# Optimization experiments

Measured on AMD Instinct MI355X. Metric: run time of the kernel, lower is better.

The kernel has to match this reference:

```python
import jax, jax.numpy as jnp
import numpy as np

B, T, H, W, C = 2, 8, 20, 36, 512
NH = 4
HD = C // NH
WS = (5, 9)
EXP = (2, 4)              # window_size // 2
KP = (5, 9)               # focal unfold kernel for level k=0
PADP = (2, 4)
T2T_K, T2T_S, T2T_P = (7, 7), (3, 3), (3, 3)
FFN_HD = 1960
NWH, NWW = H // WS[0], W // WS[1]   # 4, 4
WAREA = WS[0] * WS[1]               # 45


def _valid_ind_rolled():
    wh, ww = WS
    eh, ew = EXP
    m = np.ones((4, wh, ww), np.float32)
    m[0, :wh - eh, :ww - ew] = 0   # tl
    m[1, :wh - eh, ew:] = 0        # tr
    m[2, eh:, :ww - ew] = 0        # bl
    m[3, eh:, ew:] = 0             # br
    return jnp.asarray(np.nonzero(m.reshape(-1))[0])

VALID_ROLLED = _valid_ind_rolled()  # (120,)


def unfold(x, k, s, p):
    # x: (N, Cc, Hh, Ww) -> (N, Cc*kh*kw, L); matches torch.nn.Unfold layout (c slowest).
    N, Cc, Hh, Ww = x.shape
    kh, kw = k; sh, sw = s; ph, pw = p
    xp = jnp.pad(x, ((0, 0), (0, 0), (ph, ph), (pw, pw)))
    oh = (Hh + 2 * ph - kh) // sh + 1
    ow = (Ww + 2 * pw - kw) // sw + 1
    cols = [xp[:, :, i:i + oh * sh:sh, j:j + ow * sw:sw]
            for i in range(kh) for j in range(kw)]
    patches = jnp.stack(cols, axis=2)            # (N, Cc, kh*kw, oh, ow)
    return patches.reshape(N, Cc * kh * kw, oh * ow)


def fold(patches, out_hw, k, s, p):
    # inverse of unfold (overlap-add), matches torch F.fold.
    N = patches.shape[0]
    kh, kw = k; sh, sw = s; ph, pw = p
    Hh, Ww = out_hw
    oh = (Hh + 2 * ph - kh) // sh + 1
    ow = (Ww + 2 * pw - kw) // sw + 1
    Cc = patches.shape[1] // (kh * kw)
    pr = patches.reshape(N, Cc, kh, kw, oh, ow)
    out = jnp.zeros((N, Cc, Hh + 2 * ph, Ww + 2 * pw), patches.dtype)
    for i in range(kh):
        for j in range(kw):
            out = out.at[:, :, i:i + oh * sh:sh, j:j + ow * sw:sw].add(pr[:, :, i, j])
    return out[:, :, ph:ph + Hh, pw:pw + Ww]


def layer_norm(x, g, b):
    mu = jnp.mean(x, -1, keepdims=True)
    var = jnp.var(x, -1, keepdims=True)
    return (x - mu) * jax.lax.rsqrt(var + 1e-5) * g + b


def win_part(x):
    # (B,T,H,W,C) -> (B*nW, T*wh*ww, C)
    b = x.shape[0]
    x = x.reshape(b, T, NWH, WS[0], NWW, WS[1], C)
    return x.transpose(0, 2, 4, 1, 3, 5, 6).reshape(-1, T * WAREA, C)


def to_heads(w):
    return w.reshape(-1, T, WAREA, NH, HD).transpose(0, 3, 1, 2, 4).reshape(-1, NH, T * WAREA, HD)


def block_forward(x, g1, be1, wqkv, bqkv, wproj, bproj, wpool, bpool, g2, be2, w1, bf1, w2, bf2, out_h, out_w):
    shortcut = x
    xn = layer_norm(x, g1, be1)

    # ---- coarser (pooled) focal level, k=0 (focal_level=2) ----
    wnr = xn.reshape(B, T, NWH, WS[0], NWW, WS[1], C).transpose(0, 2, 4, 1, 3, 5, 6)
    wnr = wnr.reshape(B, NWH, NWW, T, WAREA, C)
    pooled = jnp.einsum('bhwtnc,n->bhwtc', wnr, wpool) + bpool   # (B,NWH,NWW,T,C)

    # ---- window attention ----
    qkv = xn @ wqkv + bqkv                                       # (B,T,H,W,3C)
    q, k, v = jnp.split(qkv, 3, axis=-1)
    qw = to_heads(win_part(q)) * (HD ** -0.5)
    kw_, vw = to_heads(win_part(k)), to_heads(win_part(v))

    def rolled(t):
        parts = []
        for sh, sw in ((-EXP[0], -EXP[1]), (-EXP[0], EXP[1]), (EXP[0], -EXP[1]), (EXP[0], EXP[1])):
            r = jnp.roll(t, (sh, sw), axis=(2, 3))
            parts.append(win_part(r).reshape(-1, T, WAREA, NH, HD))
        cat = jnp.concatenate(parts, axis=2)                     # (B*nW, T, 4*warea, NH, HD)
        cat = jnp.take(cat.transpose(0, 3, 1, 2, 4), VALID_ROLLED, axis=3)
        return cat.reshape(-1, NH, T * VALID_ROLLED.shape[0], HD)

    k_rolled = jnp.concatenate([kw_, rolled(k)], axis=2)         # (B*nW, NH, T*165, HD)
    v_rolled = jnp.concatenate([vw, rolled(v)], axis=2)

    # pooled keys/values via focal unfold
    xp = pooled.transpose(0, 3, 1, 2, 4)                          # (B,T,NWH,NWW,C)
    qkv_p = xp @ wqkv + bqkv
    kp, vp = qkv_p[..., C:2 * C], qkv_p[..., 2 * C:]

    def unfold_kv(t):
        t = t.transpose(0, 1, 4, 2, 3).reshape(B * T, C, NWH, NWW)
        u = unfold(t, KP, (1, 1), PADP)                           # (B*T, C*45, L)
        L = u.shape[-1]
        u = u.reshape(B, T, C, KP[0], KP[1], L).transpose(0, 5, 1, 3, 4, 2)
        u = u.reshape(B * L, T, KP[0] * KP[1], NH, HD).transpose(0, 3, 1, 2, 4)
        return u.reshape(B * L, NH, T * KP[0] * KP[1], HD)

    k_all = jnp.concatenate([k_rolled, unfold_kv(kp)], axis=2)
    v_all = jnp.concatenate([v_rolled, unfold_kv(vp)], axis=2)

    attn = jnp.einsum('wnqd,wnkd->wnqk', qw, k_all)               # (B*nW, NH, T*45, N)

    # validity mask for pooled context (zero-padded unfold positions -> -100)
    ones = jnp.ones((T, 1, NWH, NWW), x.dtype)
    um = unfold(ones, KP, (1, 1), PADP)                           # (T, 45, L)
    L = um.shape[-1]
    mvals = jnp.where(um.reshape(T, KP[0] * KP[1], L).transpose(2, 0, 1).reshape(L, -1) == 0,
                      jnp.asarray(-100.0, x.dtype), jnp.asarray(0.0, x.dtype))
    n_rolled = k_rolled.shape[2]
    mask_cols = jnp.concatenate([jnp.zeros((L, n_rolled), x.dtype), mvals], axis=1)
    attn = attn + jnp.tile(mask_cols, (B, 1))[:, None, None, :]

    attn = jax.nn.softmax(attn, axis=-1)
    out = jnp.einsum('wnqk,wnkd->wnqd', attn, v_all)
    out = out.transpose(0, 2, 1, 3).reshape(-1, T * WAREA, C) @ wproj + bproj

    # window reverse + residual
    out = out.reshape(B, NWH, NWW, T, WS[0], WS[1], C)
    out = out.transpose(0, 3, 1, 4, 2, 5, 6).reshape(B, T, H, W, C)
    x = shortcut + out

    # ---- FusionFeedForward (fold/unfold re-normalized MLP) ----
    y = layer_norm(x, g2, be2).reshape(B, T * H * W, C)
    h = y @ w1 + bf1                                              # (B, n, 1960)
    nvec = ((out_h + 2 * T2T_P[0] - T2T_K[0]) // T2T_S[0] + 1) * \
           ((out_w + 2 * T2T_P[1] - T2T_K[1]) // T2T_S[1] + 1)
    bt = (B * T * H * W) // nvec
    norm_p = jnp.ones((bt, T2T_K[0] * T2T_K[1], nvec), x.dtype)
    norm_f = fold(norm_p, (out_h, out_w), T2T_K, T2T_S, T2T_P)    # (bt,1,out_h,out_w)
    h_f = fold(h.reshape(bt, nvec, FFN_HD).transpose(0, 2, 1), (out_h, out_w), T2T_K, T2T_S, T2T_P)
    h = unfold(h_f / norm_f, T2T_K, T2T_S, T2T_P).transpose(0, 2, 1).reshape(B, T * H * W, FFN_HD)
    h = jax.nn.gelu(h, approximate=False) @ w2 + bf2
    return x + h.reshape(B, T, H, W, C)


def setup_inputs() -> dict:
    key = jax.random.key(0)
    ks = jax.random.split(key, 8)
    s = 0.02
    return dict(
        x=jax.random.normal(ks[0], (B, T, H, W, C), jnp.float32),
        g1=jnp.ones((C,), jnp.float32),
        be1=jnp.zeros((C,), jnp.float32),
        wqkv=jax.random.normal(ks[1], (C, 3 * C), jnp.float32) * s,
        bqkv=jnp.zeros((3 * C,), jnp.float32),
        wproj=jax.random.normal(ks[2], (C, C), jnp.float32) * s,
        bproj=jnp.zeros((C,), jnp.float32),
        wpool=jnp.full((WAREA,), 1.0 / WAREA, jnp.float32),
        bpool=jnp.zeros((1,), jnp.float32),
        g2=jnp.ones((C,), jnp.float32),
        be2=jnp.zeros((C,), jnp.float32),
        w1=jax.random.normal(ks[3], (C, FFN_HD), jnp.float32) * s,
        bf1=jnp.zeros((FFN_HD,), jnp.float32),
        w2=jax.random.normal(ks[4], (FFN_HD, C), jnp.float32) * s,
        bf2=jnp.zeros((C,), jnp.float32),
        out_h=60,
        out_w=108,
    )


def reference(x, g1, be1, wqkv, bqkv, wproj, bproj, wpool, bpool, g2, be2, w1, bf1, w2, bf2, out_h, out_w):
    return block_forward(x, g1, be1, wqkv, bqkv, wproj, bproj, wpool, bpool,
                         g2, be2, w1, bf1, w2, bf2, out_h, out_w)
```

## Files before the change

### kernel.cpp

```cpp
#include <hip/hip_runtime.h>
#include <hip/hip_bf16.h>
#include <math.h>

typedef __hip_bfloat16 bf16;
typedef __attribute__((ext_vector_type(8))) short bf16x8;
typedef __attribute__((ext_vector_type(4))) float f32x4;

#define DEVI __device__ __forceinline__

#define C_ 512
#define NH_ 4
#define NTOK 11520
#define NKEY 1680
#define NRK 120
#define FFN_ 1960
#define POOLED_FLAG 0x40000000

DEVI float bfu(unsigned u) { return __uint_as_float(u << 16); }
DEVI float ldf(const bf16* p) { return __bfloat162float(*p); }
DEVI float ldf(const float* p) { return *p; }
DEVI void stw(bf16* p, float v) { *p = __float2bfloat16(v); }
DEVI void stw(float* p, float v) { *p = v; }
DEVI unsigned short f2bs(float f) { bf16 h = __float2bfloat16(f); return *(unsigned short*)&h; }
DEVI unsigned pk2(float a, float b) {
  return (unsigned)f2bs(a) | ((unsigned)f2bs(b) << 16);
}

template <int DT> DEVI float ldw(const void* p, size_t i) {
  if (DT == 0) return __bfloat162float(((const bf16*)p)[i]);
  else         return ((const float*)p)[i];
}

DEVI void gload_lds16(const void* g, void* l) {
  __builtin_amdgcn_global_load_lds(
      (const __attribute__((address_space(1))) void*)g,
      (__attribute__((address_space(3))) void*)l, 16, 0, 0);
}

__global__ void k_detect(const void* __restrict__ g1, int* __restrict__ flag) {
  if (threadIdx.x == 0) {
    const unsigned short* p = (const unsigned short*)g1;
    *flag = (p[0] == 0x3F80u) ? 0 : 1;
  }
}

__global__ void k_prep(int* __restrict__ table) {
  if (threadIdx.x == 0) {
    int cnt = 0;
    for (int p = 0; p < 4; p++)
      for (int wi = 0; wi < 5; wi++)
        for (int wj = 0; wj < 9; wj++) {
          bool invalid;
          if (p == 0)      invalid = (wi < 3) && (wj < 5);
          else if (p == 1) invalid = (wi < 3) && (wj >= 4);
          else if (p == 2) invalid = (wi >= 2) && (wj < 5);
          else             invalid = (wi >= 2) && (wj >= 4);
          if (!invalid) table[cnt++] = p * 45 + wi * 9 + wj;
        }
  }
}

__global__ void k_ksrc(const int* __restrict__ vtab, int* __restrict__ ksrc) {
  int idx = blockIdx.x * 256 + threadIdx.x;
  if (idx >= 32 * NKEY) return;
  int w = idx / NKEY, j = idx % NKEY;
  int b = w >> 4, nh = (w >> 2) & 3, nw = w & 3;
  int val;
  if (j < 360) {
    int t = j / 45, pos = j % 45, wi = pos / 9, wj2 = pos % 9;
    val = ((b * 8 + t) * 20 + nh * 5 + wi) * 36 + nw * 9 + wj2;
  } else if (j < 1320) {
    int jj = j - 360;
    int t = jj / 120, r = jj % 120;
    int id = vtab[r];
    int p = id / 45, pos = id % 45, wi = pos / 9, wj2 = pos % 9;
    int sh = (p < 2) ? -2 : 2;
    int sw = (p & 1) ? 4 : -4;
    int hh = nh * 5 + wi - sh;
    if (hh < 0) hh += 20; else if (hh >= 20) hh -= 20;
    int ww2 = nw * 9 + wj2 - sw;
    if (ww2 < 0) ww2 += 36; else if (ww2 >= 36) ww2 -= 36;
    val = ((b * 8 + t) * 20 + hh) * 36 + ww2;
  } else {
    int jj = j - 1320;
    int t = jj / 45, kidx = jj % 45, ki = kidx / 9, kj = kidx % 9;
    int snh = nh + ki - 2, snw = nw + kj - 4;
    if (snh < 0 || snh >= 4 || snw < 0 || snw >= 4) val = -1;
    else val = POOLED_FLAG | ((b * 8 + t) * 16 + snh * 4 + snw);
  }
  ksrc[idx] = val;
}

template <int DT>
__global__ void k_wcvt(const int* __restrict__ dflag, const void* __restrict__ in,
                       bf16* __restrict__ out, int K, int N, int Npad) {
  if (*dflag != DT) return;
  int idx = blockIdx.x * 256 + threadIdx.x;
  if (idx >= Npad * K) return;
  int n = idx / K, k = idx % K;
  float v = (n < N) ? ldw<DT>(in, (size_t)k * N + n) : 0.f;
  out[idx] = __float2bfloat16(v);
}

template <int DT>
__global__ void k_bcvt(const int* __restrict__ dflag, const void* __restrict__ in,
                       float* __restrict__ out, int n) {
  if (*dflag != DT) return;
  int i = blockIdx.x * 256 + threadIdx.x;
  if (i < n) out[i] = ldw<DT>(in, i);
}

template <int DT, typename InT>
__global__ void k_ln(const int* __restrict__ dflag, const InT* __restrict__ xin,
                     const void* __restrict__ g, const void* __restrict__ be,
                     bf16* __restrict__ out) {
  if (*dflag != DT) return;
  const int tok = blockIdx.x;
  const int tid = threadIdx.x;
  const size_t base = (size_t)tok * C_;
  float v0 = ldf(xin + base + tid);
  float v1 = ldf(xin + base + tid + 256);
  float s = v0 + v1, ss = v0 * v0 + v1 * v1;
#pragma unroll
  for (int o = 32; o; o >>= 1) { s += __shfl_xor(s, o); ss += __shfl_xor(ss, o); }
  __shared__ float sh[10];
  const int lane = tid & 63, wv = tid >> 6;
  if (lane == 0) { sh[wv] = s; sh[4 + wv] = ss; }
  __syncthreads();
  if (tid == 0) {
    float a = sh[0] + sh[1] + sh[2] + sh[3];
    float q = sh[4] + sh[5] + sh[6] + sh[7];
    float mu = a * (1.0f / C_);
    float var = q * (1.0f / C_) - mu * mu;
    sh[8] = mu; sh[9] = rsqrtf(fmaxf(var, 0.f) + 1e-5f);
  }
  __syncthreads();
  float mu = sh[8], inv = sh[9];
  stw(out + base + tid,
      (v0 - mu) * inv * ldw<DT>(g, tid) + ldw<DT>(be, tid));
  stw(out + base + tid + 256,
      (v1 - mu) * inv * ldw<DT>(g, tid + 256) + ldw<DT>(be, tid + 256));
}

template <int DT>
__global__ void k_pool(const int* __restrict__ dflag, const bf16* __restrict__ xn,
                       const void* __restrict__ wpool, const void* __restrict__ bpool,
                       float* __restrict__ pooled) {
  if (*dflag != DT) return;
  int idx = blockIdx.x * blockDim.x + threadIdx.x;
  if (idx >= 256 * C_) return;
  int c = idx & (C_ - 1);
  int fw = idx >> 9;
  int nw = fw & 3, nh = (fw >> 2) & 3;
  int bt = fw >> 4;
  float acc = ldw<DT>(bpool, 0);
  for (int wi = 0; wi < 5; wi++) {
    int hh = nh * 5 + wi;
    const bf16* base = xn + (((size_t)(bt * 20 + hh)) * 36 + nw * 9) * C_ + c;
    for (int wj = 0; wj < 9; wj++)
      acc += __bfloat162float(base[(size_t)wj * C_]) * ldw<DT>(wpool, wi * 9 + wj);
  }
  pooled[idx] = acc;
}

template <int DT>
__global__ void k_gemm_small(const int* __restrict__ dflag, const float* __restrict__ A,
                             const void* __restrict__ Bw, const void* __restrict__ bias,
                             float* __restrict__ Cc) {
  if (*dflag != DT) return;
  int n = blockIdx.x * blockDim.x + threadIdx.x;
  int m = blockIdx.y;
  if (n >= 1536) return;
  float acc = ldw<DT>(bias, n);
  const float* a = A + (size_t)m * C_;
  for (int k = 0; k < C_; k++)
    acc += a[k] * ldw<DT>(Bw, (size_t)k * 1536 + n);
  Cc[(size_t)m * 1536 + n] = acc;
}

template <int DT, int RES, typename OutT>
__global__ __launch_bounds__(256) void k_gemm_m(const int* __restrict__ dflag,
                                                const bf16* __restrict__ A,
                                                const bf16* __restrict__ Bt,
                                                const float* __restrict__ bias,
                                                const void* __restrict__ resid,
                                                OutT* __restrict__ out,
                                                int M, int N, int K) {
  if (dflag && *dflag != DT) return;
  __shared__ __align__(16) unsigned short As[128 * 32];
  __shared__ __align__(16) unsigned short Bs[128 * 32];
  const int tid = threadIdx.x;
  const int lane = tid & 63, wid = tid >> 6;
  const int r15 = lane & 15, quad = lane >> 4;
  const int wm = wid >> 1, wn = wid & 1;
  const int m0 = blockIdx.y * 128, n0 = blockIdx.x * 128;

  f32x4 acc[4][4];
#pragma unroll
  for (int i = 0; i < 4; i++)
#pragma unroll
    for (int j = 0; j < 4; j++)
#pragma unroll
      for (int e = 0; e < 4; e++) acc[i][j][e] = 0.f;

  const int lrow = lane >> 2, lcol = (lane & 3) * 8;

  for (int k0 = 0; k0 < K; k0 += 32) {
    int rem = K - k0;
    if (rem >= 32) {
      const bf16* ga = A + (size_t)(m0 + wid * 32 + lrow) * K + k0 + lcol;
      gload_lds16(ga, &As[wid * 1024]);
      gload_lds16(ga + (size_t)16 * K, &As[wid * 1024 + 512]);
      const bf16* gb = Bt + (size_t)(n0 + wid * 32 + lrow) * K + k0 + lcol;
      gload_lds16(gb, &Bs[wid * 1024]);
      gload_lds16(gb + (size_t)16 * K, &Bs[wid * 1024 + 512]);
    } else {
      int r = tid >> 2, c = (tid & 3) * 8;
      uint4 z = make_uint4(0, 0, 0, 0);
      uint4 a0 = z, a1 = z, b0 = z, b1 = z;
      if (c < rem) {
        a0 = *(const uint4*)(A + (size_t)(m0 + r) * K + k0 + c);
        a1 = *(const uint4*)(A + (size_t)(m0 + r + 64) * K + k0 + c);
        b0 = *(const uint4*)(Bt + (size_t)(n0 + r) * K + k0 + c);
        b1 = *(const uint4*)(Bt + (size_t)(n0 + r + 64) * K + k0 + c);
      }
      *(uint4*)&As[r * 32 + c] = a0;
      *(uint4*)&As[(r + 64) * 32 + c] = a1;
      *(uint4*)&Bs[r * 32 + c] = b0;
      *(uint4*)&Bs[(r + 64) * 32 + c] = b1;
    }
    __syncthreads();

    bf16x8 af[4], bfr[4];
#pragma unroll
    for (int mf = 0; mf < 4; mf++)
      af[mf] = *(const bf16x8*)&As[(wm * 64 + mf * 16 + r15) * 32 + quad * 8];
#pragma unroll
    for (int nf = 0; nf < 4; nf++)
      bfr[nf] = *(const bf16x8*)&Bs[(wn * 64 + nf * 16 + r15) * 32 + quad * 8];
#pragma unroll
    for (int mf = 0; mf < 4; mf++)
#pragma unroll
      for (int nf = 0; nf < 4; nf++)
        acc[mf][nf] = __builtin_amdgcn_mfma_f32_16x16x32_bf16(af[mf], bfr[nf],
                                                              acc[mf][nf], 0, 0, 0);
    __syncthreads();
  }

#pragma unroll
  for (int nf = 0; nf < 4; nf++) {
    int n = n0 + wn * 64 + nf * 16 + r15;
    if (n >= N) continue;
    float bv = bias[n];
#pragma unroll
    for (int mf = 0; mf < 4; mf++) {
      int mb = m0 + wm * 64 + mf * 16 + quad * 4;
#pragma unroll
      for (int e = 0; e < 4; e++) {
        size_t off = (size_t)(mb + e) * N + n;
        float v = acc[mf][nf][e] + bv;
        if (RES == 1) v += ldw<DT>(resid, off);
        else if (RES == 2) v += ((const float*)resid)[off];
        stw(out + off, v);
      }
    }
  }
}

#define KT 64
#define KPAD 136
#define VPAD 72
__global__ __launch_bounds__(256) void k_attn_m(const bf16* __restrict__ qkv,
                                                const float* __restrict__ qkvp,
                                                const int* __restrict__ ksrc,
                                                bf16* __restrict__ ao) {
  __shared__ int ks_l[NKEY];
  __shared__ __align__(16) unsigned short ktl[KT * KPAD];
  __shared__ __align__(16) unsigned short vtl[128 * VPAD];
  __shared__ __align__(16) unsigned short ptl[4 * 16 * VPAD];
  __shared__ float maskv[KT];

  const int tid = threadIdx.x;
  const int lane = tid & 63, wid = tid >> 6;
  const int r15 = lane & 15, quad = lane >> 4;
  const int w = blockIdx.x, qt = blockIdx.y, n = blockIdx.z;
  const int b = w >> 4, nh = (w >> 2) & 3, nw = w & 3;
  const unsigned short* qkvs = (const unsigned short*)qkv;

  for (int j = tid; j < NKEY; j += 256) ks_l[j] = ksrc[w * NKEY + j];

  bf16x8 qf[4];
  {
    int qw = qt * 64 + wid * 16 + r15;
    int qc2 = qw < 360 ? qw : 359;
    int t = qc2 / 45, pos = qc2 % 45, wi = pos / 9, wj = pos % 9;
    int tok = ((b * 8 + t) * 20 + nh * 5 + wi) * 36 + nw * 9 + wj;
    const unsigned short* qp = qkvs + (size_t)tok * 1536 + n * 128 + quad * 8;
#pragma unroll
    for (int c = 0; c < 4; c++)
      qf[c] = *(const bf16x8*)(qp + c * 32);
  }

  f32x4 of[8];
#pragma unroll
  for (int nt = 0; nt < 8; nt++)
#pragma unroll
    for (int e = 0; e < 4; e++) of[nt][e] = 0.f;
  float m_[4], l_[4];
#pragma unroll
  for (int e = 0; e < 4; e++) { m_[e] = -1e30f; l_[e] = 0.f; }

  unsigned short* ptw = &ptl[wid * 16 * VPAD];
  __syncthreads();

  const int kr = tid >> 2, kp = tid & 3;
  const int vr = lane, vp = wid;
  uint4 kreg[4], vreg[4];
  float mreg = -30000.f;

  auto load_tile = [&](int j0) {
    int cnt = NKEY - j0; if (cnt > KT) cnt = KT;
    {
      int s0 = (kr < cnt) ? ks_l[j0 + kr] : -1;
      mreg = (s0 < 0) ? -30000.f : 0.f;
      if (s0 < 0) {
        kreg[0] = kreg[1] = kreg[2] = kreg[3] = make_uint4(0, 0, 0, 0);
      } else if (s0 & POOLED_FLAG) {
        const float* kf = qkvp + (size_t)(s0 & 0x3FFFFFFF) * 1536 + 512 + n * 128 + kp * 32;
#pragma unroll
        for (int i = 0; i < 4; i++) {
          float4 f0 = ((const float4*)kf)[2 * i], f1 = ((const float4*)kf)[2 * i + 1];
          kreg[i] = make_uint4(pk2(f0.x, f0.y), pk2(f0.z, f0.w),
                               pk2(f1.x, f1.y), pk2(f1.z, f1.w));
        }
      } else {
        const uint4* kq = (const uint4*)(qkvs + (size_t)s0 * 1536 + 512 + n * 128 + kp * 32);
#pragma unroll
        for (int i = 0; i < 4; i++) kreg[i] = kq[i];
      }
    }
    {
      int s1 = (vr < cnt) ? ks_l[j0 + vr] : -1;
      if (s1 < 0) {
        vreg[0] = vreg[1] = vreg[2] = vreg[3] = make_uint4(0, 0, 0, 0);
      } else if (s1 & POOLED_FLAG) {
        const float* vf = qkvp + (size_t)(s1 & 0x3FFFFFFF) * 1536 + 1024 + n * 128 + vp * 32;
#pragma unroll
        for (int i = 0; i < 4; i++) {
          float4 f0 = ((const float4*)vf)[2 * i], f1 = ((const float4*)vf)[2 * i + 1];
          vreg[i] = make_uint4(pk2(f0.x, f0.y), pk2(f0.z, f0.w),
                               pk2(f1.x, f1.y), pk2(f1.z, f1.w));
        }
      } else {
        const uint4* vq = (const uint4*)(qkvs + (size_t)s1 * 1536 + 1024 + n * 128 + vp * 32);
#pragma unroll
        for (int i = 0; i < 4; i++) vreg[i] = vq[i];
      }
    }
  };

  auto store_tile = [&]() {
    if (kp == 0) maskv[kr] = mreg;
#pragma unroll
    for (int i = 0; i < 4; i++)
      *(uint4*)&ktl[kr * KPAD + kp * 32 + i * 8] = kreg[i];
#pragma unroll
    for (int i = 0; i < 4; i++) {
      uint4 u = vreg[i];
      int d0 = vp * 32 + i * 8;
      vtl[(d0 + 0) * VPAD + vr] = (unsigned short)(u.x & 0xFFFFu);
      vtl[(d0 + 1) * VPAD + vr] = (unsigned short)(u.x >> 16);
      vtl[(d0 + 2) * VPAD + vr] = (unsigned short)(u.y & 0xFFFFu);
      vtl[(d0 + 3) * VPAD + vr] = (unsigned short)(u.y >> 16);
      vtl[(d0 + 4) * VPAD + vr] = (unsigned short)(u.z & 0xFFFFu);
      vtl[(d0 + 5) * VPAD + vr] = (unsigned short)(u.z >> 16);
      vtl[(d0 + 6) * VPAD + vr] = (unsigned short)(u.w & 0xFFFFu);
      vtl[(d0 + 7) * VPAD + vr] = (unsigned short)(u.w >> 16);
    }
  };

  load_tile(0);
  store_tile();
  __syncthreads();

  int j0 = 0;
  while (true) {
    int nxt = j0 + KT;
    if (nxt < NKEY) load_tile(nxt);

    f32x4 sf[4];
#pragma unroll
    for (int ft = 0; ft < 4; ft++)
#pragma unroll
      for (int e = 0; e < 4; e++) sf[ft][e] = 0.f;
#pragma unroll
    for (int kc = 0; kc < 4; kc++) {
      bf16x8 a = qf[kc];
#pragma unroll
      for (int ft = 0; ft < 4; ft++) {
        bf16x8 bb = *(const bf16x8*)&ktl[(ft * 16 + r15) * KPAD + kc * 32 + quad * 8];
        sf[ft] = __builtin_amdgcn_mfma_f32_16x16x32_bf16(a, bb, sf[ft], 0, 0, 0);
      }
    }
    const float scl = 0.088388347648318447f;
#pragma unroll
    for (int ft = 0; ft < 4; ft++) {
      float mk = maskv[ft * 16 + r15];
#pragma unroll
      for (int e = 0; e < 4; e++) sf[ft][e] = sf[ft][e] * scl + mk;
    }
    float tm[4], rs[4];
#pragma unroll
    for (int e = 0; e < 4; e++) {
      float v = fmaxf(fmaxf(sf[0][e], sf[1][e]), fmaxf(sf[2][e], sf[3][e]));
#pragma unroll
      for (int o = 1; o < 16; o <<= 1) v = fmaxf(v, __shfl_xor(v, o));
      tm[e] = v;
    }
#pragma unroll
    for (int e = 0; e < 4; e++) {
      float mn = fmaxf(m_[e], tm[e]);
      float alpha = __expf(m_[e] - mn);
      m_[e] = mn;
      rs[e] = 0.f;
#pragma unroll
      for (int ft = 0; ft < 4; ft++) {
        float pv = __expf(sf[ft][e] - mn);
        rs[e] += pv;
        ptw[(quad * 4 + e) * VPAD + ft * 16 + r15] = f2bs(pv);
      }
#pragma unroll
      for (int o = 1; o < 16; o <<= 1) rs[e] += __shfl_xor(rs[e], o);
      l_[e] = l_[e] * alpha + rs[e];
#pragma unroll
      for (int nt = 0; nt < 8; nt++) of[nt][e] *= alpha;
    }
#pragma unroll
    for (int kc = 0; kc < 2; kc++) {
      bf16x8 pa = *(const bf16x8*)&ptw[r15 * VPAD + kc * 32 + quad * 8];
#pragma unroll
      for (int nt = 0; nt < 8; nt++) {
        bf16x8 vb = *(const bf16x8*)&vtl[(nt * 16 + r15) * VPAD + kc * 32 + quad * 8];
        of[nt] = __builtin_amdgcn_mfma_f32_16x16x32_bf16(pa, vb, of[nt], 0, 0, 0);
      }
    }

    if (nxt >= NKEY) break;
    __syncthreads();
    store_tile();
    __syncthreads();
    j0 = nxt;
  }

#pragma unroll
  for (int e = 0; e < 4; e++) {
    int qw = qt * 64 + wid * 16 + quad * 4 + e;
    if (qw >= 360) continue;
    float inv = 1.0f / l_[e];
    int t = qw / 45, pos = qw % 45, wi = pos / 9, wj = pos % 9;
    int tok = ((b * 8 + t) * 20 + nh * 5 + wi) * 36 + nw * 9 + wj;
    bf16* op = ao + (size_t)tok * 512 + n * 128 + r15;
#pragma unroll
    for (int nt = 0; nt < 8; nt++)
      stw(op + nt * 16, of[nt][e] * inv);
  }
}

__global__ void k_fold(const bf16* __restrict__ h1, float* __restrict__ hf) {
  int idx = blockIdx.x * 256 + threadIdx.x;
  if (idx >= 16 * 40 * 60 * 108) return;
  int x = idx % 108;
  int tmp = idx / 108;
  int y = tmp % 60; tmp /= 60;
  int c = tmp % 40;
  int bt = tmp / 40;
  float sum = 0.f;
  int cnt = 0;
  for (int ki = y % 3; ki < 7; ki += 3) {
    int num = y + 3 - ki;
    if (num < 0) continue;
    int oh = num / 3;
    if (oh >= 20) continue;
    for (int kj = x % 3; kj < 7; kj += 3) {
      int num2 = x + 3 - kj;
      if (num2 < 0) continue;
      int ow = num2 / 3;
      if (ow >= 36) continue;
      sum += __bfloat162float(
          h1[(size_t)(bt * 720 + oh * 36 + ow) * FFN_ + c * 49 + ki * 7 + kj]);
      cnt++;
    }
  }
  hf[idx] = sum / (float)cnt;
}

__global__ void k_unfold_gelu(const float* __restrict__ hf, bf16* __restrict__ h2) {
  int idx = blockIdx.x * 256 + threadIdx.x;
  if (idx >= NTOK * FFN_) return;
  int f = idx % FFN_;
  int token = idx / FFN_;
  int c = f / 49, k = f % 49, ki = k / 7, kj = k % 7;
  int bt = token / 720, vec = token % 720;
  int oh = vec / 36, ow = vec % 36;
  int y = oh * 3 + ki - 3, x = ow * 3 + kj - 3;
  float v = 0.f;
  if (y >= 0 && y < 60 && x >= 0 && x < 108)
    v = hf[((size_t)(bt * 40 + c) * 60 + y) * 108 + x];
  float g = 0.5f * v * (1.0f + erff(v * 0.70710678118654752f));
  stw(h2 + idx, g);
}

extern "C" void kernel_launch(void* const* d_in, const int* in_sizes, int n_in,
                              void* d_out, int out_size, void* d_ws, size_t ws_size,
                              hipStream_t stream) {
  (void)in_sizes; (void)n_in; (void)out_size; (void)ws_size;
  const void* x     = d_in[0];
  const void* g1    = d_in[1];
  const void* be1   = d_in[2];
  const void* wqkv  = d_in[3];
  const void* bqkv  = d_in[4];
  const void* wproj = d_in[5];
  const void* bproj = d_in[6];
  const void* wpool = d_in[7];
  const void* bpool = d_in[8];
  const void* g2    = d_in[9];
  const void* be2   = d_in[10];
  const void* w1    = d_in[11];
  const void* bf1   = d_in[12];
  const void* w2    = d_in[13];
  const void* bf2   = d_in[14];

  char* ws = (char*)d_ws;
  size_t off = 0;
  auto alloc = [&](size_t bytes) -> void* {
    void* p = ws + off;
    off += (bytes + 255) & ~(size_t)255;
    return p;
  };

  int*   dflag  = (int*)  alloc(256);
  int*   vtab   = (int*)  alloc(NRK * sizeof(int));
  int*   ksrc   = (int*)  alloc((size_t)32 * NKEY * sizeof(int));
  bf16*  buf2   = (bf16*) alloc((size_t)NTOK * FFN_ * 2);
  float* pooled = (float*)alloc((size_t)256 * C_ * 4);
  float* qkvp   = (float*)alloc((size_t)256 * 1536 * 4);
  float* x2     = (float*)alloc((size_t)NTOK * C_ * 4);
  float* hf     = (float*)alloc((size_t)16 * 40 * 60 * 108 * 4);
  bf16*  wqkv_t = (bf16*) alloc((size_t)1536 * 512 * 2);
  bf16*  wproj_t= (bf16*) alloc((size_t)512 * 512 * 2);
  bf16*  w1_t   = (bf16*) alloc((size_t)2048 * 512 * 2);
  bf16*  w2_t   = (bf16*) alloc((size_t)512 * FFN_ * 2);
  float* bqkv_f = (float*)alloc(1536 * 4);
  float* bproj_f= (float*)alloc(512 * 4);
  float* bf1_f  = (float*)alloc(FFN_ * 4);
  float* bf2_f  = (float*)alloc(512 * 4);

  bf16* buf1 = (bf16*)d_out;
  bf16* xn = buf1;
  bf16* ao = buf1;
  bf16* y  = buf1;
  bf16* qkv = buf2;
  bf16* h1  = buf2;

  k_detect<<<1, 64, 0, stream>>>(g1, dflag);
  k_prep<<<1, 64, 0, stream>>>(vtab);
  k_ksrc<<<(32 * NKEY) / 256, 256, 0, stream>>>(vtab, ksrc);

  k_wcvt<0><<<(1536 * 512) / 256, 256, 0, stream>>>(dflag, wqkv, wqkv_t, 512, 1536, 1536);
  k_wcvt<1><<<(1536 * 512) / 256, 256, 0, stream>>>(dflag, wqkv, wqkv_t, 512, 1536, 1536);
  k_wcvt<0><<<(512 * 512) / 256, 256, 0, stream>>>(dflag, wproj, wproj_t, 512, 512, 512);
  k_wcvt<1><<<(512 * 512) / 256, 256, 0, stream>>>(dflag, wproj, wproj_t, 512, 512, 512);
  k_wcvt<0><<<(2048 * 512) / 256, 256, 0, stream>>>(dflag, w1, w1_t, 512, FFN_, 2048);
  k_wcvt<1><<<(2048 * 512) / 256, 256, 0, stream>>>(dflag, w1, w1_t, 512, FFN_, 2048);
  k_wcvt<0><<<(512 * FFN_ + 255) / 256, 256, 0, stream>>>(dflag, w2, w2_t, FFN_, 512, 512);
  k_wcvt<1><<<(512 * FFN_ + 255) / 256, 256, 0, stream>>>(dflag, w2, w2_t, FFN_, 512, 512);
  k_bcvt<0><<<6, 256, 0, stream>>>(dflag, bqkv, bqkv_f, 1536);
  k_bcvt<1><<<6, 256, 0, stream>>>(dflag, bqkv, bqkv_f, 1536);
  k_bcvt<0><<<2, 256, 0, stream>>>(dflag, bproj, bproj_f, 512);
  k_bcvt<1><<<2, 256, 0, stream>>>(dflag, bproj, bproj_f, 512);
  k_bcvt<0><<<8, 256, 0, stream>>>(dflag, bf1, bf1_f, FFN_);
  k_bcvt<1><<<8, 256, 0, stream>>>(dflag, bf1, bf1_f, FFN_);
  k_bcvt<0><<<2, 256, 0, stream>>>(dflag, bf2, bf2_f, 512);
  k_bcvt<1><<<2, 256, 0, stream>>>(dflag, bf2, bf2_f, 512);

  k_ln<0, bf16><<<NTOK, 256, 0, stream>>>(dflag, (const bf16*)x, g1, be1, xn);
  k_ln<1, float><<<NTOK, 256, 0, stream>>>(dflag, (const float*)x, g1, be1, xn);

  k_pool<0><<<512, 256, 0, stream>>>(dflag, xn, wpool, bpool, pooled);
  k_pool<1><<<512, 256, 0, stream>>>(dflag, xn, wpool, bpool, pooled);

  k_gemm_m<0, 0, bf16><<<dim3(12, 90), 256, 0, stream>>>(
      nullptr, xn, wqkv_t, bqkv_f, nullptr, qkv, NTOK, 1536, 512);

  k_gemm_small<0><<<dim3(6, 256), 256, 0, stream>>>(dflag, pooled, wqkv, bqkv, qkvp);
  k_gemm_small<1><<<dim3(6, 256), 256, 0, stream>>>(dflag, pooled, wqkv, bqkv, qkvp);

  k_attn_m<<<dim3(32, 6, NH_), 256, 0, stream>>>(qkv, qkvp, ksrc, ao);

  k_gemm_m<0, 1, float><<<dim3(4, 90), 256, 0, stream>>>(
      dflag, ao, wproj_t, bproj_f, x, x2, NTOK, 512, 512);
  k_gemm_m<1, 1, float><<<dim3(4, 90), 256, 0, stream>>>(
      dflag, ao, wproj_t, bproj_f, x, x2, NTOK, 512, 512);

  k_ln<0, float><<<NTOK, 256, 0, stream>>>(dflag, x2, g2, be2, y);
  k_ln<1, float><<<NTOK, 256, 0, stream>>>(dflag, x2, g2, be2, y);

  k_gemm_m<0, 0, bf16><<<dim3(16, 90), 256, 0, stream>>>(
      nullptr, y, w1_t, bf1_f, nullptr, h1, NTOK, FFN_, 512);

  k_fold<<<(16 * 40 * 60 * 108) / 256, 256, 0, stream>>>(h1, hf);

  k_unfold_gelu<<<(NTOK * FFN_) / 256, 256, 0, stream>>>(hf, h1);

  k_gemm_m<0, 2, bf16><<<dim3(4, 90), 256, 0, stream>>>(
      dflag, h1, w2_t, bf2_f, x2, (bf16*)d_out, NTOK, 512, FFN_);
  k_gemm_m<1, 2, float><<<dim3(4, 90), 256, 0, stream>>>(
      dflag, h1, w2_t, bf2_f, x2, (float*)d_out, NTOK, 512, FFN_);
}
```

Baseline: 636.4 us.

## Merge dtype-duplicated launches, tile weight transpose, use 64x64 GEMM for N=512

Replaces the per-dtype template kernel pairs with single kernels that branch on the runtime dtype flag, which roughly halves the number of launches. Weight conversion becomes one batched kernel that transposes through a shared-memory tile, so both global reads and writes are coalesced, and bias conversion becomes one kernel. The two N=512 GEMMs (proj and FFN down) move to a new 64x64-tile MFMA kernel with four times as many blocks, to fill the CUs better. The cost is runtime branching in the store path and less data reuse per block in the smaller-tile GEMM.

```diff
diff --git a/kernel.cpp b/kernel.cpp
--- a/kernel.cpp
+++ b/kernel.cpp
@@ -17,18 +17,13 @@
 #define POOLED_FLAG 0x40000000
 
 DEVI float bfu(unsigned u) { return __uint_as_float(u << 16); }
-DEVI float ldf(const bf16* p) { return __bfloat162float(*p); }
-DEVI float ldf(const float* p) { return *p; }
 DEVI void stw(bf16* p, float v) { *p = __float2bfloat16(v); }
-DEVI void stw(float* p, float v) { *p = v; }
 DEVI unsigned short f2bs(float f) { bf16 h = __float2bfloat16(f); return *(unsigned short*)&h; }
 DEVI unsigned pk2(float a, float b) {
   return (unsigned)f2bs(a) | ((unsigned)f2bs(b) << 16);
 }
-
-template <int DT> DEVI float ldw(const void* p, size_t i) {
-  if (DT == 0) return __bfloat162float(((const bf16*)p)[i]);
-  else         return ((const float*)p)[i];
+DEVI float ldwr(const void* p, size_t i, int dt) {
+  return dt ? ((const float*)p)[i] : __bfloat162float(((const bf16*)p)[i]);
 }
 
 DEVI void gload_lds16(const void* g, void* l) {
@@ -91,35 +86,66 @@
   ksrc[idx] = val;
 }
 
-template <int DT>
-__global__ void k_wcvt(const int* __restrict__ dflag, const void* __restrict__ in,
-                       bf16* __restrict__ out, int K, int N, int Npad) {
-  if (*dflag != DT) return;
-  int idx = blockIdx.x * 256 + threadIdx.x;
-  if (idx >= Npad * K) return;
-  int n = idx / K, k = idx % K;
-  float v = (n < N) ? ldw<DT>(in, (size_t)k * N + n) : 0.f;
-  out[idx] = __float2bfloat16(v);
-}
-
-template <int DT>
-__global__ void k_bcvt(const int* __restrict__ dflag, const void* __restrict__ in,
-                       float* __restrict__ out, int n) {
-  if (*dflag != DT) return;
+__global__ void k_wcvt_all(const int* __restrict__ dflag,
+                           const void* __restrict__ w0, const void* __restrict__ w1i,
+                           const void* __restrict__ w2i, const void* __restrict__ w3i,
+                           bf16* __restrict__ o0, bf16* __restrict__ o1,
+                           bf16* __restrict__ o2, bf16* __restrict__ o3) {
+  __shared__ unsigned short tile[64][65];
+  const int dt = *dflag;
+  int bid = blockIdx.x;
+  const void* in; bf16* out; int K, N, nn;
+  if (bid < 192)      { in = w0;  out = o0; K = 512;  N = 1536; nn = 24; }
+  else if (bid < 256) { in = w1i; out = o1; K = 512;  N = 512;  nn = 8;  bid -= 192; }
+  else if (bid < 512) { in = w2i; out = o2; K = 512;  N = 1960; nn = 32; bid -= 256; }
+  else                { in = w3i; out = o3; K = 1960; N = 512;  nn = 8;  bid -= 512; }
+  int tn = bid % nn, tk = bid / nn;
+  int n0 = tn * 64, k0 = tk * 64;
+  int cr = threadIdx.x >> 6;
+  int cc = threadIdx.x & 63;
+#pragma unroll
+  for (int p = 0; p < 16; p++) {
+    int kr = p * 4 + cr;
+    float v = 0.f;
+    if (k0 + kr < K && n0 + cc < N)
+      v = ldwr(in, (size_t)(k0 + kr) * N + n0 + cc, dt);
+    tile[kr][cc] = f2bs(v);
+  }
+  __syncthreads();
+#pragma unroll
+  for (int p = 0; p < 16; p++) {
+    int nr = p * 4 + cr;
+    int k = k0 + cc;
+    if (k < K) {
+      unsigned short u = tile[cc][nr];
+      out[(size_t)(n0 + nr) * K + k] = *(bf16*)&u;
+    }
+  }
+}
+
+__global__ void k_bcvt_all(const int* __restrict__ dflag,
+                           const void* __restrict__ b0, const void* __restrict__ b1,
+                           const void* __restrict__ b2, const void* __restrict__ b3,
+                           float* __restrict__ o0, float* __restrict__ o1,
+                           float* __restrict__ o2, float* __restrict__ o3) {
+  const int dt = *dflag;
   int i = blockIdx.x * 256 + threadIdx.x;
-  if (i < n) out[i] = ldw<DT>(in, i);
-}
-
-template <int DT, typename InT>
-__global__ void k_ln(const int* __restrict__ dflag, const InT* __restrict__ xin,
-                     const void* __restrict__ g, const void* __restrict__ be,
-                     bf16* __restrict__ out) {
-  if (*dflag != DT) return;
+  if (i < 1536)      o0[i] = ldwr(b0, i, dt);
+  else if (i < 2048) o1[i - 1536] = ldwr(b1, i - 1536, dt);
+  else if (i < 4008) o2[i - 2048] = ldwr(b2, i - 2048, dt);
+  else if (i < 4520) o3[i - 4008] = ldwr(b3, i - 4008, dt);
+}
+
+__global__ void k_ln(const int* __restrict__ dflag, int xmode,
+                     const void* __restrict__ xin, const void* __restrict__ g,
+                     const void* __restrict__ be, bf16* __restrict__ out) {
+  const int dt = *dflag;
+  const int xf32 = xmode | dt;
   const int tok = blockIdx.x;
   const int tid = threadIdx.x;
   const size_t base = (size_t)tok * C_;
-  float v0 = ldf(xin + base + tid);
-  float v1 = ldf(xin + base + tid + 256);
+  float v0 = ldwr(xin, base + tid, xf32);
+  float v1 = ldwr(xin, base + tid + 256, xf32);
   float s = v0 + v1, ss = v0 * v0 + v1 * v1;
 #pragma unroll
   for (int o = 32; o; o >>= 1) { s += __shfl_xor(s, o); ss += __shfl_xor(ss, o); }
@@ -137,56 +163,63 @@
   __syncthreads();
   float mu = sh[8], inv = sh[9];
   stw(out + base + tid,
-      (v0 - mu) * inv * ldw<DT>(g, tid) + ldw<DT>(be, tid));
+      (v0 - mu) * inv * ldwr(g, tid, dt) + ldwr(be, tid, dt));
   stw(out + base + tid + 256,
-      (v1 - mu) * inv * ldw<DT>(g, tid + 256) + ldw<DT>(be, tid + 256));
-}
-
-template <int DT>
+      (v1 - mu) * inv * ldwr(g, tid + 256, dt) + ldwr(be, tid + 256, dt));
+}
+
 __global__ void k_pool(const int* __restrict__ dflag, const bf16* __restrict__ xn,
                        const void* __restrict__ wpool, const void* __restrict__ bpool,
                        float* __restrict__ pooled) {
-  if (*dflag != DT) return;
+  const int dt = *dflag;
   int idx = blockIdx.x * blockDim.x + threadIdx.x;
   if (idx >= 256 * C_) return;
   int c = idx & (C_ - 1);
   int fw = idx >> 9;
   int nw = fw & 3, nh = (fw >> 2) & 3;
   int bt = fw >> 4;
-  float acc = ldw<DT>(bpool, 0);
+  float acc = ldwr(bpool, 0, dt);
   for (int wi = 0; wi < 5; wi++) {
     int hh = nh * 5 + wi;
     const bf16* base = xn + (((size_t)(bt * 20 + hh)) * 36 + nw * 9) * C_ + c;
     for (int wj = 0; wj < 9; wj++)
-      acc += __bfloat162float(base[(size_t)wj * C_]) * ldw<DT>(wpool, wi * 9 + wj);
+      acc += __bfloat162float(base[(size_t)wj * C_]) * ldwr(wpool, wi * 9 + wj, dt);
   }
   pooled[idx] = acc;
 }
 
-template <int DT>
 __global__ void k_gemm_small(const int* __restrict__ dflag, const float* __restrict__ A,
                              const void* __restrict__ Bw, const void* __restrict__ bias,
                              float* __restrict__ Cc) {
-  if (*dflag != DT) return;
+  const int dt = *dflag;
   int n = blockIdx.x * blockDim.x + threadIdx.x;
   int m = blockIdx.y;
   if (n >= 1536) return;
-  float acc = ldw<DT>(bias, n);
+  float acc = ldwr(bias, n, dt);
   const float* a = A + (size_t)m * C_;
   for (int k = 0; k < C_; k++)
-    acc += a[k] * ldw<DT>(Bw, (size_t)k * 1536 + n);
+    acc += a[k] * ldwr(Bw, (size_t)k * 1536 + n, dt);
   Cc[(size_t)m * 1536 + n] = acc;
 }
 
-template <int DT, int RES, typename OutT>
+DEVI void gemm_store(int dt, int resmode, int outmode, const void* resid, void* out,
+                     size_t off, float v) {
+  if (resmode)
+    v += ((resmode == 2) || dt) ? ((const float*)resid)[off]
+                                : __bfloat162float(((const bf16*)resid)[off]);
+  if ((outmode == 1) || (outmode == 2 && dt)) ((float*)out)[off] = v;
+  else ((bf16*)out)[off] = __float2bfloat16(v);
+}
+
 __global__ __launch_bounds__(256) void k_gemm_m(const int* __restrict__ dflag,
+                                                int resmode, int outmode,
                                                 const bf16* __restrict__ A,
                                                 const bf16* __restrict__ Bt,
                                                 const float* __restrict__ bias,
                                                 const void* __restrict__ resid,
-                                                OutT* __restrict__ out,
+                                                void* __restrict__ out,
                                                 int M, int N, int K) {
-  if (dflag && *dflag != DT) return;
+  const int dt = *dflag;
   __shared__ __align__(16) unsigned short As[128 * 32];
   __shared__ __align__(16) unsigned short Bs[128 * 32];
   const int tid = threadIdx.x;
@@ -258,10 +291,87 @@
 #pragma unroll
       for (int e = 0; e < 4; e++) {
         size_t off = (size_t)(mb + e) * N + n;
-        float v = acc[mf][nf][e] + bv;
-        if (RES == 1) v += ldw<DT>(resid, off);
-        else if (RES == 2) v += ((const float*)resid)[off];
-        stw(out + off, v);
+        gemm_store(dt, resmode, outmode, resid, out, off, acc[mf][nf][e] + bv);
+      }
+    }
+  }
+}
+
+__global__ __launch_bounds__(256) void k_gemm_s64(const int* __restrict__ dflag,
+                                                  int resmode, int outmode,
+                                                  const bf16* __restrict__ A,
+                                                  const bf16* __restrict__ Bt,
+                                                  const float* __restrict__ bias,
+                                                  const void* __restrict__ resid,
+                                                  void* __restrict__ out,
+                                                  int M, int N, int K) {
+  const int dt = *dflag;
+  __shared__ __align__(16) unsigned short As[64 * 32];
+  __shared__ __align__(16) unsigned short Bs[64 * 32];
+  const int tid = threadIdx.x;
+  const int lane = tid & 63, wid = tid >> 6;
+  const int r15 = lane & 15, quad = lane >> 4;
+  const int wm = wid >> 1, wn = wid & 1;
+  const int m0 = blockIdx.y * 64, n0 = blockIdx.x * 64;
+
+  f32x4 acc[2][2];
+#pragma unroll
+  for (int i = 0; i < 2; i++)
+#pragma unroll
+    for (int j = 0; j < 2; j++)
+#pragma unroll
+      for (int e = 0; e < 4; e++) acc[i][j][e] = 0.f;
+
+  const int lrow = lane >> 2, lcol = (lane & 3) * 8;
+
+  for (int k0 = 0; k0 < K; k0 += 32) {
+    int rem = K - k0;
+    if (rem >= 32) {
+      const bf16* ga = A + (size_t)(m0 + wid * 16 + lrow) * K + k0 + lcol;
+      gload_lds16(ga, &As[wid * 512]);
+      const bf16* gb = Bt + (size_t)(n0 + wid * 16 + lrow) * K + k0 + lcol;
+      gload_lds16(gb, &Bs[wid * 512]);
+    } else {
+      int r = tid >> 2, c = (tid & 3) * 8;
+      uint4 z = make_uint4(0, 0, 0, 0);
+      uint4 a0 = z, b0 = z;
+      if (c < rem) {
+        a0 = *(const uint4*)(A + (size_t)(m0 + r) * K + k0 + c);
+        b0 = *(const uint4*)(Bt + (size_t)(n0 + r) * K + k0 + c);
+      }
+      *(uint4*)&As[r * 32 + c] = a0;
+      *(uint4*)&Bs[r * 32 + c] = b0;
+    }
+    __syncthreads();
+
+    bf16x8 af[2], bfr[2];
+#pragma unroll
+    for (int mf = 0; mf < 2; mf++)
+      af[mf] = *(const bf16x8*)&As[(wm * 32 + mf * 16 + r15) * 32 + quad * 8];
+#pragma unroll
+    for (int nf = 0; nf < 2; nf++)
+      bfr[nf] = *(const bf16x8*)&Bs[(wn * 32 + nf * 16 + r15) * 32 + quad * 8];
+#pragma unroll
+    for (int mf = 0; mf < 2; mf++)
+#pragma unroll
+      for (int nf = 0; nf < 2; nf++)
+        acc[mf][nf] = __builtin_amdgcn_mfma_f32_16x16x32_bf16(af[mf], bfr[nf],
+                                                              acc[mf][nf], 0, 0, 0);
+    __syncthreads();
+  }
+
+#pragma unroll
+  for (int nf = 0; nf < 2; nf++) {
+    int n = n0 + wn * 32 + nf * 16 + r15;
+    if (n >= N) continue;
+    float bv = bias[n];
+#pragma unroll
+    for (int mf = 0; mf < 2; mf++) {
+      int mb = m0 + wm * 32 + mf * 16 + quad * 4;
+#pragma unroll
+      for (int e = 0; e < 4; e++) {
+        size_t off = (size_t)(mb + e) * N + n;
+        gemm_store(dt, resmode, outmode, resid, out, off, acc[mf][nf][e] + bv);
       }
     }
   }
@@ -566,54 +676,34 @@
   k_prep<<<1, 64, 0, stream>>>(vtab);
   k_ksrc<<<(32 * NKEY) / 256, 256, 0, stream>>>(vtab, ksrc);
 
-  k_wcvt<0><<<(1536 * 512) / 256, 256, 0, stream>>>(dflag, wqkv, wqkv_t, 512, 1536, 1536);
-  k_wcvt<1><<<(1536 * 512) / 256, 256, 0, stream>>>(dflag, wqkv, wqkv_t, 512, 1536, 1536);
-  k_wcvt<0><<<(512 * 512) / 256, 256, 0, stream>>>(dflag, wproj, wproj_t, 512, 512, 512);
-  k_wcvt<1><<<(512 * 512) / 256, 256, 0, stream>>>(dflag, wproj, wproj_t, 512, 512, 512);
-  k_wcvt<0><<<(2048 * 512) / 256, 256, 0, stream>>>(dflag, w1, w1_t, 512, FFN_, 2048);
-  k_wcvt<1><<<(2048 * 512) / 256, 256, 0, stream>>>(dflag, w1, w1_t, 512, FFN_, 2048);
-  k_wcvt<0><<<(512 * FFN_ + 255) / 256, 256, 0, stream>>>(dflag, w2, w2_t, FFN_, 512, 512);
-  k_wcvt<1><<<(512 * FFN_ + 255) / 256, 256, 0, stream>>>(dflag, w2, w2_t, FFN_, 512, 512);
-  k_bcvt<0><<<6, 256, 0, stream>>>(dflag, bqkv, bqkv_f, 1536);
-  k_bcvt<1><<<6, 256, 0, stream>>>(dflag, bqkv, bqkv_f, 1536);
-  k_bcvt<0><<<2, 256, 0, stream>>>(dflag, bproj, bproj_f, 512);
-  k_bcvt<1><<<2, 256, 0, stream>>>(dflag, bproj, bproj_f, 512);
-  k_bcvt<0><<<8, 256, 0, stream>>>(dflag, bf1, bf1_f, FFN_);
-  k_bcvt<1><<<8, 256, 0, stream>>>(dflag, bf1, bf1_f, FFN_);
-  k_bcvt<0><<<2, 256, 0, stream>>>(dflag, bf2, bf2_f, 512);
-  k_bcvt<1><<<2, 256, 0, stream>>>(dflag, bf2, bf2_f, 512);
-
-  k_ln<0, bf16><<<NTOK, 256, 0, stream>>>(dflag, (const bf16*)x, g1, be1, xn);
-  k_ln<1, float><<<NTOK, 256, 0, stream>>>(dflag, (const float*)x, g1, be1, xn);
-
-  k_pool<0><<<512, 256, 0, stream>>>(dflag, xn, wpool, bpool, pooled);
-  k_pool<1><<<512, 256, 0, stream>>>(dflag, xn, wpool, bpool, pooled);
-
-  k_gemm_m<0, 0, bf16><<<dim3(12, 90), 256, 0, stream>>>(
-      nullptr, xn, wqkv_t, bqkv_f, nullptr, qkv, NTOK, 1536, 512);
-
-  k_gemm_small<0><<<dim3(6, 256), 256, 0, stream>>>(dflag, pooled, wqkv, bqkv, qkvp);
-  k_gemm_small<1><<<dim3(6, 256), 256, 0, stream>>>(dflag, pooled, wqkv, bqkv, qkvp);
+  k_wcvt_all<<<760, 256, 0, stream>>>(dflag, wqkv, wproj, w1, w2,
+                                      wqkv_t, wproj_t, w1_t, w2_t);
+  k_bcvt_all<<<18, 256, 0, stream>>>(dflag, bqkv, bproj, bf1, bf2,
+                                     bqkv_f, bproj_f, bf1_f, bf2_f);
+
+  k_ln<<<NTOK, 256, 0, stream>>>(dflag, 0, x, g1, be1, xn);
+
+  k_pool<<<512, 256, 0, stream>>>(dflag, xn, wpool, bpool, pooled);
+
+  k_gemm_m<<<dim3(12, 90), 256, 0, stream>>>(
+      dflag, 0, 0, xn, wqkv_t, bqkv_f, nullptr, qkv, NTOK, 1536, 512);
+
+  k_gemm_small<<<dim3(6, 256), 256, 0, stream>>>(dflag, pooled, wqkv, bqkv, qkvp);
 
   k_attn_m<<<dim3(32, 6, NH_), 256, 0, stream>>>(qkv, qkvp, ksrc, ao);
 
-  k_gemm_m<0, 1, float><<<dim3(4, 90), 256, 0, stream>>>(
-      dflag, ao, wproj_t, bproj_f, x, x2, NTOK, 512, 512);
-  k_gemm_m<1, 1, float><<<dim3(4, 90), 256, 0, stream>>>(
-      dflag, ao, wproj_t, bproj_f, x, x2, NTOK, 512, 512);
-
-  k_ln<0, float><<<NTOK, 256, 0, stream>>>(dflag, x2, g2, be2, y);
-  k_ln<1, float><<<NTOK, 256, 0, stream>>>(dflag, x2, g2, be2, y);
-
-  k_gemm_m<0, 0, bf16><<<dim3(16, 90), 256, 0, stream>>>(
-      nullptr, y, w1_t, bf1_f, nullptr, h1, NTOK, FFN_, 512);
+  k_gemm_s64<<<dim3(8, 180), 256, 0, stream>>>(
+      dflag, 1, 1, ao, wproj_t, bproj_f, x, x2, NTOK, 512, 512);
+
+  k_ln<<<NTOK, 256, 0, stream>>>(dflag, 1, x2, g2, be2, y);
+
+  k_gemm_m<<<dim3(16, 90), 256, 0, stream>>>(
+      dflag, 0, 0, y, w1_t, bf1_f, nullptr, h1, NTOK, FFN_, 512);
 
   k_fold<<<(16 * 40 * 60 * 108) / 256, 256, 0, stream>>>(h1, hf);
 
   k_unfold_gelu<<<(NTOK * FFN_) / 256, 256, 0, stream>>>(hf, h1);
 
-  k_gemm_m<0, 2, bf16><<<dim3(4, 90), 256, 0, stream>>>(
-      dflag, h1, w2_t, bf2_f, x2, (bf16*)d_out, NTOK, 512, FFN_);
-  k_gemm_m<1, 2, float><<<dim3(4, 90), 256, 0, stream>>>(
-      dflag, h1, w2_t, bf2_f, x2, (float*)d_out, NTOK, 512, FFN_);
-}
+  k_gemm_s64<<<dim3(8, 180), 256, 0, stream>>>(
+      dflag, 2, 2, h1, w2_t, bf2_f, x2, d_out, NTOK, 512, FFN_);
+}
```

After: 654.2 us. 2.8% more time.
